# Performance work log

Measured on AMD Instinct MI355X. Metric: run time of the kernel, lower is better.

## Reference

```python
import jax, jax.numpy as jnp
import numpy as np

B, S, D_IN, D_OUT = 8, 2048, 1024, 1024


def setup_inputs() -> dict:
    key = jax.random.key(0)
    ks = jax.random.split(key, 9)
    sc = 1.0 / np.sqrt(D_IN)
    return {
        "in_k": jax.random.normal(ks[0], (B, S, D_IN), jnp.float32),
        "in_q": jax.random.normal(ks[1], (B, S, D_IN), jnp.float32),
        "in_v": jax.random.normal(ks[2], (B, S, D_IN), jnp.float32),
        "Wk": jax.random.normal(ks[3], (D_IN, D_OUT), jnp.float32) * sc,
        "bk": jax.random.normal(ks[4], (D_OUT,), jnp.float32) * sc,
        "Wq": jax.random.normal(ks[5], (D_IN, D_OUT), jnp.float32) * sc,
        "bq": jax.random.normal(ks[6], (D_OUT,), jnp.float32) * sc,
        "Wv": jax.random.normal(ks[7], (D_IN, D_OUT), jnp.float32) * sc,
        "bv": jax.random.normal(ks[8], (D_OUT,), jnp.float32) * sc,
    }


def reference(in_k, in_q, in_v, Wk, bk, Wq, bq, Wv, bv):
    k = in_k @ Wk + bk  # [B,S,D]
    q = in_q @ Wq + bq
    v = in_v @ Wv + bv
    scale = 1.0 / jnp.sqrt(jnp.asarray(D_OUT, q.dtype))
    scores = jnp.einsum("bqd,bkd->bqk", q, k) * scale  # [B,S,S]
    attn = jax.nn.softmax(scores, axis=-1)
    return jnp.einsum("bqk,bkd->bqd", attn, v)
```

## Files before the change

### kernel.cpp

```cpp
#include <hip/hip_runtime.h>
#include <hip/hip_bf16.h>
#include <stdint.h>

typedef __bf16 bf16x8 __attribute__((ext_vector_type(8)));
typedef float  f32x4  __attribute__((ext_vector_type(4)));
typedef uint16_t u16x8 __attribute__((ext_vector_type(8)));

__device__ __forceinline__ uint16_t f32_to_bf16(float f) {
    union { float f; uint32_t u; } v; v.f = f;
    uint32_t u = v.u;
    uint32_t r = (u + 0x7FFFu + ((u >> 16) & 1u)) >> 16;
    return (uint16_t)r;
}

__device__ __forceinline__ void gld16(const void* g, void* l) {
    __builtin_amdgcn_global_load_lds(
        (const __attribute__((address_space(1))) void*)g,
        (__attribute__((address_space(3))) void*)l,
        16, 0, 0);
}

#define MFMA16 __builtin_amdgcn_mfma_f32_16x16x32_bf16
#define SBAR   __builtin_amdgcn_s_barrier
#define SCHED0() __builtin_amdgcn_sched_barrier(0)
#define PRIO   __builtin_amdgcn_s_setprio

__global__ __launch_bounds__(256) void cast3_kernel(
    const float* __restrict__ i0, const float* __restrict__ i1,
    const float* __restrict__ i2, uint16_t* __restrict__ o0,
    uint16_t* __restrict__ o1, uint16_t* __restrict__ o2) {
    const float* in = (blockIdx.z == 0) ? i0 : (blockIdx.z == 1) ? i1 : i2;
    uint16_t* out = (blockIdx.z == 0) ? o0 : (blockIdx.z == 1) ? o1 : o2;
    size_t i = ((size_t)blockIdx.x * 256 + threadIdx.x) * 8;
    float4 a = *(const float4*)(in + i);
    float4 b = *(const float4*)(in + i + 4);
    u16x8 o;
    o[0] = f32_to_bf16(a.x); o[1] = f32_to_bf16(a.y);
    o[2] = f32_to_bf16(a.z); o[3] = f32_to_bf16(a.w);
    o[4] = f32_to_bf16(b.x); o[5] = f32_to_bf16(b.y);
    o[6] = f32_to_bf16(b.z); o[7] = f32_to_bf16(b.w);
    *(u16x8*)(out + i) = o;
}

__global__ __launch_bounds__(256) void wtrans_kernel(
    const float* __restrict__ W0, const float* __restrict__ W1,
    const float* __restrict__ W2, uint16_t* __restrict__ Wt0) {
    const float* W = (blockIdx.z == 0) ? W0 : (blockIdx.z == 1) ? W1 : W2;
    uint16_t* Wt = Wt0 + (size_t)blockIdx.z * 1024 * 1024;
    __shared__ float tile[64][65];
    const int n0 = blockIdx.x * 64, k0 = blockIdx.y * 64;
    const int tx = threadIdx.x & 63, ty0 = threadIdx.x >> 6;
#pragma unroll
    for (int r = 0; r < 16; ++r) {
        int ty = ty0 + r * 4;
        tile[ty][tx] = W[(size_t)(k0 + ty) * 1024 + n0 + tx];
    }
    __syncthreads();
#pragma unroll
    for (int r = 0; r < 16; ++r) {
        int ty = ty0 + r * 4;
        Wt[(size_t)(n0 + ty) * 1024 + k0 + tx] = f32_to_bf16(tile[tx][ty]);
    }
}

__device__ __forceinline__ void stage_tile(const uint16_t* __restrict__ G,
                                           int ldg, int k0,
                                           uint16_t* lds, int tid) {
    const int r = tid >> 3, ch = tid & 7;
    const int c = ((ch ^ (r & 7)) << 3);
#pragma unroll
    for (int i = 0; i < 4; ++i) {
        const int row = i * 64 + r;
        gld16(G + (size_t)row * ldg + k0 + c, lds + i * 4096 + tid * 8);
    }
}

__device__ __forceinline__ void gemm_core(const uint16_t* __restrict__ A, int lda,
                                          const uint16_t* __restrict__ B, int ldb,
                                          int K, f32x4 (&acc)[8][4]) {
    __shared__ __align__(16) uint16_t As[2][16384];
    __shared__ __align__(16) uint16_t Bs[2][16384];
    const int tid  = threadIdx.x;
    const int lane = tid & 63;
    const int wave = tid >> 6;
    const int wr = wave >> 2, wcn = wave & 3;
    const int mrow = lane & 15, q = lane >> 4;
    const int sx = mrow & 7;
    const int abase = (wr * 128 + mrow) * 64;
    const int bbase = (wcn * 64 + mrow) * 64;
    const int c0 = ((q ^ sx) << 3);
    const int c1 = (((4 + q) ^ sx) << 3);

    stage_tile(A, lda, 0, As[0], tid);
    stage_tile(B, ldb, 0, Bs[0], tid);
    __syncthreads();

    const int NT = K >> 6;
    bf16x8 af[4][2], bA[2][2], bB[2][2];
    for (int t = 0; t < NT; ++t) {
        const int cur = t & 1;
        const uint16_t* as = As[cur];
        const uint16_t* bs = Bs[cur];
        const int kn = (t + 1) << 6;
        const bool pf = (t + 1 < NT);

        if (pf) stage_tile(A, lda, kn, As[cur ^ 1], tid);
#pragma unroll
        for (int m = 0; m < 4; ++m) {
            af[m][0] = *(const bf16x8*)&as[abase + m * 1024 + c0];
            af[m][1] = *(const bf16x8*)&as[abase + m * 1024 + c1];
        }
#pragma unroll
        for (int n = 0; n < 2; ++n) {
            bA[n][0] = *(const bf16x8*)&bs[bbase + n * 1024 + c0];
            bA[n][1] = *(const bf16x8*)&bs[bbase + n * 1024 + c1];
        }
        SBAR(); SCHED0();
        PRIO(1);
#pragma unroll
        for (int m = 0; m < 4; ++m)
#pragma unroll
            for (int n = 0; n < 2; ++n) {
                acc[m][n] = MFMA16(af[m][0], bA[n][0], acc[m][n], 0, 0, 0);
                acc[m][n] = MFMA16(af[m][1], bA[n][1], acc[m][n], 0, 0, 0);
            }
        PRIO(0);
        SBAR(); SCHED0();

        if (pf) stage_tile(B, ldb, kn, Bs[cur ^ 1], tid);
#pragma unroll
        for (int n = 0; n < 2; ++n) {
            bB[n][0] = *(const bf16x8*)&bs[bbase + (n + 2) * 1024 + c0];
            bB[n][1] = *(const bf16x8*)&bs[bbase + (n + 2) * 1024 + c1];
        }
        SBAR(); SCHED0();
        PRIO(1);
#pragma unroll
        for (int m = 0; m < 4; ++m)
#pragma unroll
            for (int n = 0; n < 2; ++n) {
                acc[m][n + 2] = MFMA16(af[m][0], bB[n][0], acc[m][n + 2], 0, 0, 0);
                acc[m][n + 2] = MFMA16(af[m][1], bB[n][1], acc[m][n + 2], 0, 0, 0);
            }
        PRIO(0);
        SBAR(); SCHED0();

#pragma unroll
        for (int m = 0; m < 4; ++m) {
            af[m][0] = *(const bf16x8*)&as[abase + (m + 4) * 1024 + c0];
            af[m][1] = *(const bf16x8*)&as[abase + (m + 4) * 1024 + c1];
        }
        SBAR(); SCHED0();
        PRIO(1);
#pragma unroll
        for (int m = 0; m < 4; ++m)
#pragma unroll
            for (int n = 0; n < 2; ++n) {
                acc[m + 4][n + 2] = MFMA16(af[m][0], bB[n][0], acc[m + 4][n + 2], 0, 0, 0);
                acc[m + 4][n + 2] = MFMA16(af[m][1], bB[n][1], acc[m + 4][n + 2], 0, 0, 0);
            }
#pragma unroll
        for (int m = 0; m < 4; ++m)
#pragma unroll
            for (int n = 0; n < 2; ++n) {
                acc[m + 4][n] = MFMA16(af[m][0], bA[n][0], acc[m + 4][n], 0, 0, 0);
                acc[m + 4][n] = MFMA16(af[m][1], bA[n][1], acc[m + 4][n], 0, 0, 0);
            }
        PRIO(0);
        __syncthreads();
    }
}

__global__ __launch_bounds__(512, 2) void proj256_kernel(
    const uint16_t* __restrict__ Ab, const uint16_t* __restrict__ Bb,
    uint16_t* __restrict__ Cb, uint16_t* __restrict__ Vt,
    const float* __restrict__ b0, const float* __restrict__ b1,
    const float* __restrict__ b2) {
    const int bid = blockIdx.x;
    const int lg = (bid & 7) * 96 + (bid >> 3);
    const int pidx = lg >> 8;
    const int t = lg & 255;
    const int band = t >> 4;
    const int Mt = band * 4 + (t & 3);
    const int Nt = (t >> 2) & 3;
    const int row0 = Mt * 256, col0 = Nt * 256;

    const uint16_t* A = Ab + (size_t)pidx * 16777216 + (size_t)row0 * 1024;
    const uint16_t* B = Bb + (size_t)pidx * 1048576 + (size_t)col0 * 1024;
    const float* bias = (pidx == 0) ? b0 : (pidx == 1) ? b1 : b2;

    f32x4 acc[8][4];
#pragma unroll
    for (int i = 0; i < 8; ++i)
#pragma unroll
        for (int j = 0; j < 4; ++j) acc[i][j] = 0.0f;

    gemm_core(A, 1024, B, 1024, 1024, acc);

    const int tid = threadIdx.x, lane = tid & 63, wave = tid >> 6;
    const int wr = wave >> 2, wcn = wave & 3;
    const int mrow = lane & 15, quad = lane >> 4;
    float bv_[4];
#pragma unroll
    for (int n = 0; n < 4; ++n) bv_[n] = bias[col0 + wcn * 64 + n * 16 + mrow];

    if (pidx < 2) {
        uint16_t* C = Cb + (size_t)pidx * 16777216;
#pragma unroll
        for (int m = 0; m < 8; ++m)
#pragma unroll
            for (int n = 0; n < 4; ++n)
#pragma unroll
                for (int r = 0; r < 4; ++r) {
                    int row = row0 + wr * 128 + m * 16 + quad * 4 + r;
                    int col = col0 + wcn * 64 + n * 16 + mrow;
                    C[(size_t)row * 1024 + col] = f32_to_bf16(acc[m][n][r] + bv_[n]);
                }
    } else {
#pragma unroll
        for (int m = 0; m < 8; ++m)
#pragma unroll
            for (int n = 0; n < 4; ++n)
#pragma unroll
                for (int r = 0; r < 4; ++r) {
                    int row = row0 + wr * 128 + m * 16 + quad * 4 + r;
                    int col = col0 + wcn * 64 + n * 16 + mrow;
                    Vt[((size_t)(row >> 11) * 1024 + col) * 2048 + (row & 2047)] =
                        f32_to_bf16(acc[m][n][r] + bv_[n]);
                }
    }
}

template <int EPI>
__global__ __launch_bounds__(512, 2) void att256_kernel(
    const uint16_t* __restrict__ Abase, int lda, long long sAz,
    const uint16_t* __restrict__ Bbase, int ldb, long long sBz,
    void* __restrict__ Cv, int ldc, long long sCz,
    int K, float alpha, float* __restrict__ sums, int NtN, int chunk) {
    const int bid = blockIdx.x;
    const int lg = (bid & 7) * chunk + (bid >> 3);
    const int z = lg / chunk;
    const int t = lg % chunk;
    const int r2 = t & (2 * NtN - 1);
    const int band = t / (2 * NtN);
    const int Mt = band * 2 + (r2 & 1);
    const int Nt = r2 >> 1;
    const int row0 = Mt * 256, col0 = Nt * 256;

    const uint16_t* A = Abase + (size_t)z * sAz + (size_t)row0 * lda;
    const uint16_t* B = Bbase + (size_t)z * sBz + (size_t)col0 * ldb;

    f32x4 acc[8][4];
#pragma unroll
    for (int i = 0; i < 8; ++i)
#pragma unroll
        for (int j = 0; j < 4; ++j) acc[i][j] = 0.0f;

    gemm_core(A, lda, B, ldb, K, acc);

    const int tid = threadIdx.x, lane = tid & 63, wave = tid >> 6;
    const int wr = wave >> 2, wcn = wave & 3;
    const int mrow = lane & 15, quad = lane >> 4;

    if (EPI == 1) {
        uint16_t* C = (uint16_t*)Cv + (size_t)z * sCz;
#pragma unroll
        for (int m = 0; m < 8; ++m)
#pragma unroll
            for (int r = 0; r < 4; ++r) {
                int row = row0 + wr * 128 + m * 16 + quad * 4 + r;
                float s = 0.0f;
#pragma unroll
                for (int n = 0; n < 4; ++n) {
                    int col = col0 + wcn * 64 + n * 16 + mrow;
                    float e = __expf(acc[m][n][r] * alpha);
                    C[(size_t)row * ldc + col] = f32_to_bf16(e);
                    s += e;
                }
                s += __shfl_xor(s, 1, 64);
                s += __shfl_xor(s, 2, 64);
                s += __shfl_xor(s, 4, 64);
                s += __shfl_xor(s, 8, 64);
                if (mrow == 0) atomicAdd(&sums[(size_t)z * 2048 + row], s);
            }
    } else {
        float* C = (float*)Cv + (size_t)z * sCz;
#pragma unroll
        for (int m = 0; m < 8; ++m)
#pragma unroll
            for (int r = 0; r < 4; ++r) {
                int row = row0 + wr * 128 + m * 16 + quad * 4 + r;
                float inv = 1.0f / sums[(size_t)z * 2048 + row];
#pragma unroll
                for (int n = 0; n < 4; ++n) {
                    int col = col0 + wcn * 64 + n * 16 + mrow;
                    C[(size_t)row * ldc + col] = acc[m][n][r] * inv;
                }
            }
    }
}

extern "C" void kernel_launch(void* const* d_in, const int* in_sizes, int n_in,
                              void* d_out, int out_size, void* d_ws, size_t ws_size,
                              hipStream_t stream) {
    const float* in_k = (const float*)d_in[0];
    const float* in_q = (const float*)d_in[1];
    const float* in_v = (const float*)d_in[2];
    const float* Wk = (const float*)d_in[3];
    const float* bk = (const float*)d_in[4];
    const float* Wq = (const float*)d_in[5];
    const float* bq = (const float*)d_in[6];
    const float* Wv = (const float*)d_in[7];
    const float* bv = (const float*)d_in[8];
    float* out = (float*)d_out;

    char* w = (char*)d_ws;
    uint16_t* Xq  = (uint16_t*)(w + 0);
    uint16_t* Xk  = (uint16_t*)(w + 33554432);
    uint16_t* Xv  = (uint16_t*)(w + 67108864);
    uint16_t* Qb  = (uint16_t*)(w + 100663296);
    uint16_t* Kb  = (uint16_t*)(w + 134217728);
    uint16_t* Vt  = (uint16_t*)(w + 167772160);
    uint16_t* Wqt = (uint16_t*)(w + 201326592);
    uint16_t* Sc  = Xq;
    float*    sums = (float*)Xv;

    wtrans_kernel<<<dim3(16, 16, 3), 256, 0, stream>>>(Wq, Wk, Wv, Wqt);
    cast3_kernel<<<dim3(8192, 1, 3), 256, 0, stream>>>(in_q, in_k, in_v, Xq, Xk, Xv);

    proj256_kernel<<<768, 512, 0, stream>>>(Xq, Wqt, Qb, Vt, bq, bk, bv);

    hipMemsetAsync(sums, 0, 8 * 2048 * sizeof(float), stream);

    att256_kernel<1><<<512, 512, 0, stream>>>(
        Qb, 1024, 2048LL * 1024, Kb, 1024, 2048LL * 1024,
        Sc, 2048, 2048LL * 2048, 1024, 0.03125f, sums, 8, 64);

    att256_kernel<2><<<256, 512, 0, stream>>>(
        Sc, 2048, 2048LL * 2048, Vt, 2048, 1024LL * 2048,
        out, 1024, 2048LL * 1024, 2048, 1.0f, sums, 4, 32);
}
```

Measured before the change: 565.2 us.

## Pipeline projection GEMM loads in quarter-tile chunks with vmcnt waits

Restructures the projection GEMM main loop so the next K-tile is staged in four quarter chunks interleaved between the MFMA phases, each gated by a partial s_waitcnt vmcnt rather than a full __syncthreads. The B tile's LDS layout is remapped so each half of the N dimension is contiguous, letting the chunks land independently. The aim is to overlap global-to-LDS traffic with compute and remove the full barrier drain at the end of every iteration. In exchange, correctness now depends on hand-counted vmcnt values and on the last iteration issuing redundant loads from offset zero.

New measurement: 517.6 us. -8.4%, faster.

```diff
diff --git a/kernel.cpp b/kernel.cpp
--- a/kernel.cpp
+++ b/kernel.cpp
@@ -24,6 +24,8 @@
 #define SBAR   __builtin_amdgcn_s_barrier
 #define SCHED0() __builtin_amdgcn_sched_barrier(0)
 #define PRIO   __builtin_amdgcn_s_setprio
+#define VMCNT4() asm volatile("s_waitcnt vmcnt(4)" ::: "memory")
+#define VMCNT0() asm volatile("s_waitcnt vmcnt(0)" ::: "memory")
 
 __global__ __launch_bounds__(256) void cast3_kernel(
     const float* __restrict__ i0, const float* __restrict__ i1,
@@ -63,16 +65,23 @@
     }
 }
 
-__device__ __forceinline__ void stage_tile(const uint16_t* __restrict__ G,
-                                           int ldg, int k0,
-                                           uint16_t* lds, int tid) {
-    const int r = tid >> 3, ch = tid & 7;
-    const int c = ((ch ^ (r & 7)) << 3);
-#pragma unroll
-    for (int i = 0; i < 4; ++i) {
-        const int row = i * 64 + r;
-        gld16(G + (size_t)row * ldg + k0 + c, lds + i * 4096 + tid * 8);
-    }
+__device__ __forceinline__ void stageA64(const uint16_t* __restrict__ G, int ldg,
+                                         int k0, int rowbase, uint16_t* ldsT, int tid) {
+    const int l = tid >> 3;
+    const int ch = tid & 7;
+    const int c = ((ch ^ (l & 7)) << 3);
+    gld16(G + (size_t)(rowbase + l) * ldg + k0 + c,
+          ldsT + (size_t)(rowbase + l) * 64 + ch * 8);
+}
+
+__device__ __forceinline__ void stageB64(const uint16_t* __restrict__ G, int ldg,
+                                         int k0, int h, int j, uint16_t* ldsT, int tid) {
+    const int lloc = j * 64 + (tid >> 3);
+    const int ch = tid & 7;
+    const int grow = (lloc & 31) + ((lloc >> 5) << 6) + (h << 5);
+    const int c = ((ch ^ (lloc & 7)) << 3);
+    gld16(G + (size_t)grow * ldg + k0 + c,
+          ldsT + (size_t)(h * 128 + lloc) * 64 + ch * 8);
 }
 
 __device__ __forceinline__ void gemm_core(const uint16_t* __restrict__ A, int lda,
@@ -86,25 +95,38 @@
     const int wr = wave >> 2, wcn = wave & 3;
     const int mrow = lane & 15, q = lane >> 4;
     const int sx = mrow & 7;
-    const int abase = (wr * 128 + mrow) * 64;
-    const int bbase = (wcn * 64 + mrow) * 64;
     const int c0 = ((q ^ sx) << 3);
     const int c1 = (((4 + q) ^ sx) << 3);
-
-    stage_tile(A, lda, 0, As[0], tid);
-    stage_tile(B, ldb, 0, Bs[0], tid);
-    __syncthreads();
+    const int abase = (wr * 128 + mrow) * 64;
+    const int bb    = (wcn * 32 + mrow) * 64;
 
     const int NT = K >> 6;
+    stageA64(A, lda, 0, 0,   As[0], tid);
+    stageA64(A, lda, 0, 128, As[0], tid);
+    SCHED0();
+    stageB64(B, ldb, 0, 0, 0, Bs[0], tid);
+    stageB64(B, ldb, 0, 0, 1, Bs[0], tid);
+    SCHED0();
+    stageB64(B, ldb, 0, 1, 0, Bs[0], tid);
+    stageB64(B, ldb, 0, 1, 1, Bs[0], tid);
+    SCHED0();
+    stageA64(A, lda, 0, 64,  As[0], tid);
+    stageA64(A, lda, 0, 192, As[0], tid);
+    SCHED0();
+
     bf16x8 af[4][2], bA[2][2], bB[2][2];
     for (int t = 0; t < NT; ++t) {
         const int cur = t & 1;
         const uint16_t* as = As[cur];
         const uint16_t* bs = Bs[cur];
-        const int kn = (t + 1) << 6;
-        const bool pf = (t + 1 < NT);
-
-        if (pf) stage_tile(A, lda, kn, As[cur ^ 1], tid);
+        uint16_t* An = As[cur ^ 1];
+        uint16_t* Bn = Bs[cur ^ 1];
+        const int kn = (t + 1 < NT) ? ((t + 1) << 6) : 0;
+
+        VMCNT4();
+        SBAR(); SCHED0();
+        stageA64(A, lda, kn, 0,   An, tid);
+        stageA64(A, lda, kn, 128, An, tid);
 #pragma unroll
         for (int m = 0; m < 4; ++m) {
             af[m][0] = *(const bf16x8*)&as[abase + m * 1024 + c0];
@@ -112,8 +134,8 @@
         }
 #pragma unroll
         for (int n = 0; n < 2; ++n) {
-            bA[n][0] = *(const bf16x8*)&bs[bbase + n * 1024 + c0];
-            bA[n][1] = *(const bf16x8*)&bs[bbase + n * 1024 + c1];
+            bA[n][0] = *(const bf16x8*)&bs[bb + n * 1024 + c0];
+            bA[n][1] = *(const bf16x8*)&bs[bb + n * 1024 + c1];
         }
         SBAR(); SCHED0();
         PRIO(1);
@@ -125,13 +147,15 @@
                 acc[m][n] = MFMA16(af[m][1], bA[n][1], acc[m][n], 0, 0, 0);
             }
         PRIO(0);
-        SBAR(); SCHED0();
-
-        if (pf) stage_tile(B, ldb, kn, Bs[cur ^ 1], tid);
+
+        VMCNT4();
+        SBAR(); SCHED0();
+        stageB64(B, ldb, kn, 0, 0, Bn, tid);
+        stageB64(B, ldb, kn, 0, 1, Bn, tid);
 #pragma unroll
         for (int n = 0; n < 2; ++n) {
-            bB[n][0] = *(const bf16x8*)&bs[bbase + (n + 2) * 1024 + c0];
-            bB[n][1] = *(const bf16x8*)&bs[bbase + (n + 2) * 1024 + c1];
+            bB[n][0] = *(const bf16x8*)&bs[bb + 8192 + n * 1024 + c0];
+            bB[n][1] = *(const bf16x8*)&bs[bb + 8192 + n * 1024 + c1];
         }
         SBAR(); SCHED0();
         PRIO(1);
@@ -143,8 +167,11 @@
                 acc[m][n + 2] = MFMA16(af[m][1], bB[n][1], acc[m][n + 2], 0, 0, 0);
             }
         PRIO(0);
-        SBAR(); SCHED0();
-
+
+        VMCNT4();
+        SBAR(); SCHED0();
+        stageB64(B, ldb, kn, 1, 0, Bn, tid);
+        stageB64(B, ldb, kn, 1, 1, Bn, tid);
 #pragma unroll
         for (int m = 0; m < 4; ++m) {
             af[m][0] = *(const bf16x8*)&as[abase + (m + 4) * 1024 + c0];
@@ -156,19 +183,26 @@
         for (int m = 0; m < 4; ++m)
 #pragma unroll
             for (int n = 0; n < 2; ++n) {
+                acc[m + 4][n] = MFMA16(af[m][0], bA[n][0], acc[m + 4][n], 0, 0, 0);
+                acc[m + 4][n] = MFMA16(af[m][1], bA[n][1], acc[m + 4][n], 0, 0, 0);
+            }
+        PRIO(0);
+
+        SBAR(); SCHED0();
+        stageA64(A, lda, kn, 64,  An, tid);
+        stageA64(A, lda, kn, 192, An, tid);
+        SBAR(); SCHED0();
+        PRIO(1);
+#pragma unroll
+        for (int m = 0; m < 4; ++m)
+#pragma unroll
+            for (int n = 0; n < 2; ++n) {
                 acc[m + 4][n + 2] = MFMA16(af[m][0], bB[n][0], acc[m + 4][n + 2], 0, 0, 0);
                 acc[m + 4][n + 2] = MFMA16(af[m][1], bB[n][1], acc[m + 4][n + 2], 0, 0, 0);
             }
-#pragma unroll
-        for (int m = 0; m < 4; ++m)
-#pragma unroll
-            for (int n = 0; n < 2; ++n) {
-                acc[m + 4][n] = MFMA16(af[m][0], bA[n][0], acc[m + 4][n], 0, 0, 0);
-                acc[m + 4][n] = MFMA16(af[m][1], bA[n][1], acc[m + 4][n], 0, 0, 0);
-            }
         PRIO(0);
-        __syncthreads();
-    }
+    }
+    VMCNT0();
 }
 
 __global__ __launch_bounds__(512, 2) void proj256_kernel(
```
